# Kernel optimization log

Measured on AMD Instinct MI355X. Metric: run time of the kernel, lower is better.

## Reference

```python
import jax, jax.numpy as jnp
import numpy as np

B, C, H, W = 4, 64, 64, 64  # x shape; mask is (B,1,8H,8W)


def _conv(x, w, pad=0):
    return jax.lax.conv_general_dilated(
        x, w, (1, 1), [(pad, pad), (pad, pad)],
        dimension_numbers=('NCHW', 'OIHW', 'NCHW'))


def _inorm(x, eps=1e-5):  # InstanceNorm2d, affine=False, biased var (torch default)
    mu = x.mean(axis=(2, 3), keepdims=True)
    var = x.var(axis=(2, 3), keepdims=True)
    return (x - mu) * jax.lax.rsqrt(var + eps)


def _forward(x, mask, kconv_w1, kconv_w2, fs_w1, fs_w2, fs_b2, fs_fuse_w):
    b, c, h, w = x.shape
    n = h * w
    # MaxPool2d(8,8) then binarize
    m = jax.lax.reduce_window(mask, -jnp.inf, jax.lax.max,
                              (1, 1, 8, 8), (1, 1, 8, 8), 'VALID')
    m = (m > 0).astype(x.dtype)
    back = 1.0 - m
    # ResidualBlock K_conv (shared for K and Q paths in original code)
    y = jax.nn.relu(_inorm(_conv(x, kconv_w1, pad=1)))
    y = _inorm(_conv(y, kconv_w2, pad=1))
    kx = jax.nn.relu(y + x)
    # L2-normalized K/Q over channel dim
    K = (kx * back).reshape(b, c, n)
    K = K / (jnp.linalg.norm(K, axis=1, keepdims=True) + 1e-8)
    Q = (kx * m).reshape(b, c, n)
    Q = Q / (jnp.linalg.norm(Q, axis=1, keepdims=True) + 1e-8)
    V = (x * back).reshape(b, c, n)
    # cosine-similarity score map, temperature 20
    score = jnp.einsum('bcq,bck->bqk', Q, K) * 20.0  # (b, n_q, n_k)
    qm = m.reshape(b, 1, n)      # query mask (foreground)
    km = back.reshape(b, 1, n)   # key mask (background)
    NEG = -1000000.0
    validx = score + (1.0 - km) * NEG + (1.0 - qm.transpose(0, 2, 1)) * NEG
    att = jax.nn.softmax(validx, axis=-1) * (qm.transpose(0, 2, 1) * km)
    # att_fore[b,c,q] = sum_k V[b,c,k] * att[b,q,k]
    att_fore = jnp.einsum('bck,bqk->bcq', V, att).reshape(b, c, h, w)
    # Fusion_score
    feat1 = _conv(jnp.concatenate([x * m, att_fore * m], axis=1), fs_w1)
    s = jax.nn.sigmoid(_conv(feat1, fs_w2) + fs_b2[None, :, None, None])
    fused = _conv(jnp.concatenate([x * m, att_fore * m * (1.0 - s)], axis=1), fs_fuse_w)
    fs_out = fused * m + x * (1.0 - m)
    out = fs_out * m + x * (1.0 - m)
    # visualization attention mask
    visatt = att.sum(axis=1).reshape(b, 1, h, w)
    attmask = jnp.repeat(jnp.repeat(visatt, 8, axis=2), 8, axis=3)  # nearest upsample x8
    attmask = attmask / attmask.max()
    return out, attmask


def setup_inputs() -> dict:
    key = jax.random.key(0)
    ks = jax.random.split(key, 8)

    def wgt(k, shape, fan_in):
        return jax.random.normal(k, shape, jnp.float32) / np.sqrt(fan_in)

    x = jax.random.normal(ks[0], (B, C, H, W), jnp.float32)
    # sparse foreground mask so maxpool(8x8)>0 yields a mixed fg/bg mask
    mask = (jax.random.uniform(ks[1], (B, 1, H * 8, W * 8)) < 0.01).astype(jnp.float32)
    return dict(
        x=x, mask=mask,
        kconv_w1=wgt(ks[2], (C, C, 3, 3), C * 9),
        kconv_w2=wgt(ks[3], (C, C, 3, 3), C * 9),
        fs_w1=wgt(ks[4], (C, 2 * C, 1, 1), 2 * C),
        fs_w2=wgt(ks[5], (C, C, 1, 1), C),
        fs_b2=jnp.zeros((C,), jnp.float32),
        fs_fuse_w=wgt(ks[6], (C, 2 * C, 1, 1), 2 * C),
    )


def reference(x, mask, kconv_w1, kconv_w2, fs_w1, fs_w2, fs_b2, fs_fuse_w):
    return _forward(x, mask, kconv_w1, kconv_w2, fs_w1, fs_w2, fs_b2, fs_fuse_w)
```

## Files before the change

### kernel.cpp

```cpp
#include <hip/hip_runtime.h>
#include <hip/hip_bf16.h>

typedef __hip_bfloat16 bf16;
typedef __attribute__((ext_vector_type(8))) short short8;
typedef __attribute__((ext_vector_type(4))) float f32x4;
typedef __attribute__((ext_vector_type(16))) float f32x16;

#define BB 4
#define CC 64
#define NN 4096
#define MH 512
#define MW 512
#define LS 72

#define WB_AFC  ((size_t)0)
#define WB_DEN  ((size_t)4194304)
#define WB_VIS  ((size_t)4259840)
#define WB_QIX  ((size_t)4325376)
#define WB_KIX  ((size_t)4390912)
#define WB_MFL  ((size_t)4456448)
#define WB_CNT  ((size_t)4472832)
#define WB_STAT ((size_t)4472896)
#define WB_WT1  ((size_t)4476992)
#define WB_WT2  ((size_t)4550720)
#define WB_WFB  ((size_t)4624448)
#define WB_XT   ((size_t)8388608)
#define WB_KXT  ((size_t)10485760)
#define WB_E    ((size_t)16777216)
#define EB_ELEM ((size_t)8388608)

__device__ __forceinline__ float b2f(bf16 v) { return __bfloat162float(v); }
__device__ __forceinline__ float us2f(unsigned short u) { return __uint_as_float(((unsigned)u) << 16); }
__device__ __forceinline__ unsigned short f2bu(float f) {
  bf16 h = __float2bfloat16(f);
  return *(unsigned short*)&h;
}

__global__ __launch_bounds__(256) void k_pre(const float* __restrict__ x,
                                             const float* __restrict__ mask,
                                             const float* __restrict__ w1,
                                             const float* __restrict__ w2,
                                             const float* __restrict__ fw1,
                                             const float* __restrict__ fw2,
                                             const float* __restrict__ fwf,
                                             float* __restrict__ outp,
                                             unsigned short* __restrict__ xt,
                                             unsigned char* __restrict__ mfl,
                                             float* __restrict__ vis,
                                             float* __restrict__ gstat,
                                             unsigned int* __restrict__ vmaxb,
                                             unsigned short* __restrict__ wT1,
                                             unsigned short* __restrict__ wT2,
                                             unsigned short* __restrict__ wfb) {
  __shared__ float lx[64][65];
  int t = threadIdx.x;
  if (blockIdx.x < 256) {
    int b = blockIdx.x >> 6, p0 = (blockIdx.x & 63) * 64;
    const float* xb = x + (size_t)b * CC * NN + p0;
    float* ob = outp + (size_t)b * CC * NN + p0;
    for (int idx = t; idx < 4096; idx += 256) {
      int c = idx >> 6, j = idx & 63;
      float v = xb[c * NN + j];
      lx[j][c] = v;
      ob[c * NN + j] = v;
    }
    __syncthreads();
    unsigned short* xo = xt + ((size_t)b * NN + p0) * 64;
    for (int idx = t; idx < 2048; idx += 256) {
      int j = idx >> 5, c2 = (idx & 31) * 2;
      ushort2 w2v;
      w2v.x = f2bu(lx[j][c2]);
      w2v.y = f2bu(lx[j][c2 + 1]);
      *(ushort2*)&xo[j * 64 + c2] = w2v;
    }
  } else {
    int g = (blockIdx.x - 256) * 256 + t;
    int o = g >> 2, sub = g & 3;
    int b = o >> 12, p = o & 4095;
    int py = p >> 6, px = p & 63;
    const float* mb = mask + (size_t)b * MH * MW + (py * 8 + sub * 2) * MW + px * 8;
    float mx = 0.f;
    #pragma unroll
    for (int dy = 0; dy < 2; ++dy) {
      const float4* r4 = (const float4*)(mb + dy * MW);
      float4 a = r4[0], c = r4[1];
      mx = fmaxf(mx, fmaxf(fmaxf(a.x, a.y), fmaxf(a.z, a.w)));
      mx = fmaxf(mx, fmaxf(fmaxf(c.x, c.y), fmaxf(c.z, c.w)));
    }
    mx = fmaxf(mx, __shfl_xor(mx, 1));
    mx = fmaxf(mx, __shfl_xor(mx, 2));
    if (sub == 0) {
      mfl[o] = (mx > 0.f) ? 1 : 0;
      vis[o] = 0.f;
    }
    if (g < 1024) gstat[g] = 0.f;
    if (g == 0) vmaxb[0] = 0u;
    if (g < 36864) {
      int tap = g >> 12;
      int rem = g & 4095;
      int co = rem >> 6, ci = rem & 63;
      int src = (co * 64 + ci) * 9 + tap;
      wT1[g] = f2bu(w1[src]);
      wT2[g] = f2bu(w2[src]);
    } else if (g < 57344) {
      int j2 = g - 36864;
      if (j2 < 8192)       wfb[j2] = f2bu(fw1[j2]);
      else if (j2 < 12288) wfb[j2] = f2bu(fw2[j2 - 8192]);
      else                 wfb[j2] = f2bu(fwf[j2 - 12288]);
    }
  }
}

__global__ __launch_bounds__(256) void k_compact(const unsigned char* __restrict__ mfl,
                                                 int* __restrict__ qidx, int* __restrict__ kidx,
                                                 int* __restrict__ nq, int* __restrict__ nk) {
  int b = blockIdx.x;
  __shared__ unsigned char lm[4096];
  int t = threadIdx.x;
  *(uint4*)&lm[t * 16] = *(const uint4*)&mfl[b * NN + t * 16];
  __syncthreads();
  if (t >= 64) return;
  int lane = t;
  int qb = 0, kb = 0;
  #pragma unroll
  for (int it = 0; it < 64; ++it) {
    int p = it * 64 + lane;
    bool f = lm[p] != 0;
    unsigned long long bal = __ballot(f);
    int before = __popcll(bal & ((1ULL << lane) - 1ULL));
    if (f)  qidx[b * NN + qb + before] = p;
    if (!f) kidx[b * NN + kb + (lane - before)] = p;
    int cnt = __popcll(bal);
    qb += cnt; kb += 64 - cnt;
  }
  if (lane == 0) { nq[b] = qb; nk[b] = kb; }
}

template <bool NORM_IN>
__global__ __launch_bounds__(256) void k_convm(const unsigned short* __restrict__ src,
                                               const unsigned short* __restrict__ wT,
                                               const float* __restrict__ insum,
                                               const float* __restrict__ insq,
                                               unsigned short* __restrict__ dst,
                                               float* __restrict__ gsum,
                                               float* __restrict__ gsq) {
  int b = blockIdx.y;
  int r = blockIdx.x;
  __shared__ unsigned short bx[198 * LS];
  __shared__ float nmean[64], ninv[64];
  int t = threadIdx.x;
  if (NORM_IN) {
    if (t < 64) {
      float m = insum[b * 64 + t] * (1.f / NN);
      float v = fmaxf(insq[b * 64 + t] * (1.f / NN) - m * m, 0.f);
      nmean[t] = m; ninv[t] = rsqrtf(v + 1e-5f);
    }
    __syncthreads();
  }
  const unsigned short* sb = src + (size_t)b * NN * 64;
  for (int idx = t; idx < 198 * 8; idx += 256) {
    int row = idx >> 3, c8 = (idx & 7) * 8;
    int dy = row / 66;
    int cx = row - dy * 66 - 1;
    int rr = r + dy - 1;
    uint4 v = make_uint4(0u, 0u, 0u, 0u);
    if ((unsigned)rr < 64u && (unsigned)cx < 64u) {
      v = *(const uint4*)(sb + ((size_t)(rr * 64 + cx)) * 64 + c8);
      if (NORM_IN) {
        unsigned short* e = (unsigned short*)&v;
        #pragma unroll
        for (int j = 0; j < 8; ++j)
          e[j] = f2bu(fmaxf((us2f(e[j]) - nmean[c8 + j]) * ninv[c8 + j], 0.f));
      }
    }
    *(uint4*)&bx[row * LS + c8] = v;
  }
  __syncthreads();
  int lane = t & 63;
  int quad = lane >> 4, col = lane & 15;
  int qw = (t >> 6) * 16;
  f32x4 acc[4] = {{0.f,0.f,0.f,0.f},{0.f,0.f,0.f,0.f},{0.f,0.f,0.f,0.f},{0.f,0.f,0.f,0.f}};
  #pragma unroll
  for (int tap = 0; tap < 9; ++tap) {
    int dy = tap / 3, dx = tap - dy * 3 - 1;
    const unsigned short* wrow = wT + ((size_t)tap * 64 + qw + col) * 64;
    short8 a0 = *(const short8*)(wrow + quad * 8);
    short8 a1 = *(const short8*)(wrow + 32 + quad * 8);
    int rbase = dy * 66 + dx + 1;
    #pragma unroll
    for (int nt = 0; nt < 4; ++nt) {
      int row = rbase + nt * 16 + col;
      short8 b0 = *(const short8*)&bx[row * LS + quad * 8];
      short8 b1 = *(const short8*)&bx[row * LS + 32 + quad * 8];
      acc[nt] = __builtin_amdgcn_mfma_f32_16x16x32_bf16(a0, b0, acc[nt], 0, 0, 0);
      acc[nt] = __builtin_amdgcn_mfma_f32_16x16x32_bf16(a1, b1, acc[nt], 0, 0, 0);
    }
  }
  #pragma unroll
  for (int rr = 0; rr < 4; ++rr) {
    float s1 = acc[0][rr] + acc[1][rr] + acc[2][rr] + acc[3][rr];
    float s2 = acc[0][rr]*acc[0][rr] + acc[1][rr]*acc[1][rr]
             + acc[2][rr]*acc[2][rr] + acc[3][rr]*acc[3][rr];
    s1 += __shfl_xor(s1, 1); s2 += __shfl_xor(s2, 1);
    s1 += __shfl_xor(s1, 2); s2 += __shfl_xor(s2, 2);
    s1 += __shfl_xor(s1, 4); s2 += __shfl_xor(s2, 4);
    s1 += __shfl_xor(s1, 8); s2 += __shfl_xor(s2, 8);
    if (col == 0) {
      int co = qw + quad * 4 + rr;
      atomicAdd(&gsum[b * 64 + co], s1);
      atomicAdd(&gsq[b * 64 + co], s2);
    }
  }
  __syncthreads();
  #pragma unroll
  for (int nt = 0; nt < 4; ++nt)
    #pragma unroll
    for (int rr = 0; rr < 4; ++rr)
      bx[(nt * 16 + col) * LS + qw + quad * 4 + rr] = f2bu(acc[nt][rr]);
  __syncthreads();
  unsigned short* db = dst + ((size_t)b * NN + r * 64) * 64;
  for (int idx = t; idx < 512; idx += 256) {
    int px = idx >> 3, c8 = (idx & 7) * 8;
    *(uint4*)(db + (size_t)px * 64 + c8) = *(const uint4*)&bx[px * LS + c8];
  }
}

__global__ __launch_bounds__(256) void k_knorm(unsigned short* __restrict__ kxt,
                                               const unsigned short* __restrict__ xt,
                                               const float* __restrict__ gsum,
                                               const float* __restrict__ gsq,
                                               float* __restrict__ afc,
                                               float* __restrict__ den) {
  int b = blockIdx.x >> 6;
  int p0 = (blockIdx.x & 63) * 64;
  __shared__ float m2[64], i2[64];
  int t = threadIdx.x;
  if (t < 64) {
    float m = gsum[b * 64 + t] * (1.f / NN);
    float v = fmaxf(gsq[b * 64 + t] * (1.f / NN) - m * m, 0.f);
    m2[t] = m; i2[t] = rsqrtf(v + 1e-5f);
  }
  size_t gid = (size_t)blockIdx.x * 256 + t;
  float4 z4 = make_float4(0.f, 0.f, 0.f, 0.f);
  float4* az = (float4*)afc;
  #pragma unroll
  for (int j = 0; j < 4; ++j) az[gid + (size_t)j * 65536] = z4;
  if (gid < 16384) den[gid] = 0.f;
  __syncthreads();
  int px = t >> 2, c0 = (t & 3) * 16;
  size_t base = ((size_t)b * NN + p0 + px) * 64 + c0;
  unsigned short kv[16], xv[16];
  *(uint4*)&kv[0] = *(const uint4*)(kxt + base);
  *(uint4*)&kv[8] = *(const uint4*)(kxt + base + 8);
  *(uint4*)&xv[0] = *(const uint4*)(xt + base);
  *(uint4*)&xv[8] = *(const uint4*)(xt + base + 8);
  float v[16]; float ss = 0.f;
  #pragma unroll
  for (int j = 0; j < 16; ++j) {
    float f = fmaxf((us2f(kv[j]) - m2[c0 + j]) * i2[c0 + j] + us2f(xv[j]), 0.f);
    v[j] = f; ss += f * f;
  }
  ss += __shfl_xor(ss, 1);
  ss += __shfl_xor(ss, 2);
  float inv = 1.f / (sqrtf(ss) + 1e-8f);
  #pragma unroll
  for (int j = 0; j < 16; ++j) kv[j] = f2bu(v[j] * inv);
  *(uint4*)(kxt + base) = *(const uint4*)&kv[0];
  *(uint4*)(kxt + base + 8) = *(const uint4*)&kv[8];
}

__global__ __launch_bounds__(256) void k_att1(const unsigned short* __restrict__ khat,
                                              const unsigned short* __restrict__ xt,
                                              const int* __restrict__ qidx, const int* __restrict__ kidx,
                                              const int* __restrict__ nqv, const int* __restrict__ nkv,
                                              float* __restrict__ afc, float* __restrict__ den,
                                              unsigned short* __restrict__ eg) {
  int b = blockIdx.y;
  int nqb = nqv[b], nkb = nkv[b];
  int q0 = (blockIdx.x >> 3) * 64;
  int part = blockIdx.x & 7;
  if (q0 >= nqb) return;
  int ntiles = (nkb + 63) >> 6;
  int nt_blk = (part < ntiles) ? ((ntiles - part + 7) >> 3) : 0;
  if (nt_blk == 0) return;
  int NKP = (nkb + 63) & ~63;
  __shared__ unsigned short lk [64 * LS];
  __shared__ unsigned short lvT[64 * LS];
  __shared__ unsigned short le [64 * LS];
  __shared__ int lidxa[512];
  int t = threadIdx.x;
  int wave = t >> 6, lane = t & 63;
  int l31 = lane & 31, lhi = lane >> 5;
  int qh = wave >> 1, kh = wave & 1;
  const int* qix = qidx + b * NN;
  const int* kix = kidx + b * NN;
  const unsigned short* khb = khat + (size_t)b * NN * 64;
  const unsigned short* xtb = xt + (size_t)b * NN * 64;
  unsigned short* egb = eg + (size_t)b * EB_ELEM;
  int qq_a = q0 + qh * 32 + l31;
  int qp_a = (qq_a < nqb) ? qix[qq_a] : qix[0];
  short8 aq[4];
  #pragma unroll
  for (int ks = 0; ks < 4; ++ks)
    aq[ks] = *(const short8*)(khb + (size_t)qp_a * 64 + ks * 16 + lhi * 8);
  for (int idx = t; idx < nt_blk * 64; idx += 256) {
    int it = idx >> 6, k = idx & 63;
    lidxa[idx] = kix[(part + it * 8) * 64 + k];
  }
  __syncthreads();
  int klo = t >> 3, c8 = (t & 7) * 8, vcc = t & 7;
  uint4 g0, g1, g2, g3;
  auto issue_gather = [&](int it) {
    int j0 = (part + it * 8) * 64;
    const int* lp = lidxa + it * 64;
    uint4 z = make_uint4(0u, 0u, 0u, 0u);
    g0 = (j0 + klo      < nkb) ? *(const uint4*)(khb + (size_t)lp[klo] * 64 + c8) : z;
    g1 = (j0 + klo + 32 < nkb) ? *(const uint4*)(khb + (size_t)lp[klo + 32] * 64 + c8) : z;
    g2 = (j0 + 2 * klo     < nkb) ? *(const uint4*)(xtb + (size_t)lp[2 * klo] * 64 + c8) : z;
    g3 = (j0 + 2 * klo + 1 < nkb) ? *(const uint4*)(xtb + (size_t)lp[2 * klo + 1] * 64 + c8) : z;
  };
  issue_gather(0);
  f32x16 pv, dsum;
  #pragma unroll
  for (int i = 0; i < 16; ++i) { pv[i] = 0.f; dsum[i] = 0.f; }
  for (int it = 0; it < nt_blk; ++it) {
    int j0 = (part + it * 8) * 64;
    __syncthreads();
    *(uint4*)&lk[klo * LS + c8] = g0;
    *(uint4*)&lk[(klo + 32) * LS + c8] = g1;
    {
      const unsigned short* e0 = (const unsigned short*)&g2;
      const unsigned short* e1 = (const unsigned short*)&g3;
      int pbase = klo & 3, prun = klo >> 2;
      int pp = pbase + ((prun ^ vcc) << 2);
      #pragma unroll
      for (int jj = 0; jj < 8; ++jj) {
        unsigned int w2 = (unsigned)e0[jj] | ((unsigned)e1[jj] << 16);
        *(unsigned int*)&lvT[(c8 + jj) * LS + pp * 2] = w2;
      }
    }
    __syncthreads();
    if (it + 1 < nt_blk) issue_gather(it + 1);
    f32x16 s;
    #pragma unroll
    for (int i = 0; i < 16; ++i) s[i] = 0.f;
    #pragma unroll
    for (int ks = 0; ks < 4; ++ks) {
      short8 bk = *(const short8*)&lk[(kh * 32 + l31) * LS + ks * 16 + lhi * 8];
      s = __builtin_amdgcn_mfma_f32_32x32x16_bf16(aq[ks], bk, s, 0, 0, 0);
    }
    bool kval = (j0 + kh * 32 + l31) < nkb;
    #pragma unroll
    for (int reg = 0; reg < 16; ++reg) {
      float e = kval ? __expf(20.f * s[reg]) : 0.f;
      dsum[reg] += e;
      int row = (reg & 3) + 8 * (reg >> 2) + 4 * lhi;
      le[(qh * 32 + row) * LS + kh * 32 + l31] = f2bu(e);
    }
    __syncthreads();
    for (int idx = t; idx < 512; idx += 256) {
      int q = idx >> 3, cc8 = (idx & 7) * 8;
      if (q0 + q < nqb)
        *(uint4*)(egb + (size_t)(q0 + q) * NKP + j0 + cc8) = *(const uint4*)&le[q * LS + cc8];
    }
    int c = kh * 32 + l31;
    int c37 = (c >> 3) & 7;
    #pragma unroll
    for (int ks = 0; ks < 4; ++ks) {
      short8 a  = *(const short8*)&le[(qh * 32 + l31) * LS + ks * 16 + lhi * 8];
      int run = ks * 2 + lhi;
      short8 bv = *(const short8*)&lvT[c * LS + ((run ^ c37) << 3)];
      pv = __builtin_amdgcn_mfma_f32_32x32x16_bf16(a, bv, pv, 0, 0, 0);
    }
  }
  #pragma unroll
  for (int reg = 0; reg < 16; ++reg) {
    float v = dsum[reg];
    v += __shfl_xor(v, 1); v += __shfl_xor(v, 2); v += __shfl_xor(v, 4);
    v += __shfl_xor(v, 8); v += __shfl_xor(v, 16);
    int row = (reg & 3) + 8 * (reg >> 2) + 4 * lhi;
    int qq = q0 + qh * 32 + row;
    if (l31 == 0 && qq < nqb) atomicAdd(&den[b * NN + qq], v);
  }
  #pragma unroll
  for (int reg = 0; reg < 16; ++reg) {
    int row = (reg & 3) + 8 * (reg >> 2) + 4 * lhi;
    int qq = q0 + qh * 32 + row;
    if (qq < nqb) atomicAdd(&afc[((size_t)b * NN + qq) * 64 + kh * 32 + l31], pv[reg]);
  }
}

__global__ __launch_bounds__(256) void k_vis(const unsigned short* __restrict__ eg,
                                             const float* __restrict__ den,
                                             const int* __restrict__ kidx,
                                             const int* __restrict__ nqv, const int* __restrict__ nkv,
                                             float* __restrict__ vis) {
  int b = blockIdx.z;
  int nqb = nqv[b], nkb = nkv[b];
  int k0 = blockIdx.x * 256;
  if (k0 >= nkb) return;
  int NKP = (nkb + 63) & ~63;
  int qpart = blockIdx.y;
  int qbeg = (qpart * nqb) >> 3;
  int qend = ((qpart + 1) * nqb) >> 3;
  __shared__ float wd[256];
  int t = threadIdx.x;
  int k = k0 + t;
  const unsigned short* eb = eg + (size_t)b * EB_ELEM;
  float acc = 0.f;
  for (int qc = qbeg; qc < qend; qc += 256) {
    __syncthreads();
    int qq = qc + t;
    float d = (qq < qend) ? den[b * NN + qq] : 0.f;
    wd[t] = (d > 0.f) ? 1.f / d : 0.f;
    __syncthreads();
    int lim = min(256, qend - qc);
    if (k < nkb) {
      const unsigned short* ep = eb + (size_t)qc * NKP + k;
      int j = 0;
      for (; j + 8 <= lim; j += 8) {
        #pragma unroll
        for (int u = 0; u < 8; ++u)
          acc += us2f(ep[(size_t)(j + u) * NKP]) * wd[j + u];
      }
      for (; j < lim; ++j)
        acc += us2f(ep[(size_t)j * NKP]) * wd[j];
    }
  }
  if (k < nkb) atomicAdd(&vis[b * NN + kidx[b * NN + k]], acc);
}

#define FS 136
__global__ __launch_bounds__(256) void k_fusionm(const unsigned short* __restrict__ xt,
                                                 const float* __restrict__ afc,
                                                 const float* __restrict__ den,
                                                 const int* __restrict__ qidx, const int* __restrict__ nqv,
                                                 const unsigned short* __restrict__ wall,
                                                 const float* __restrict__ b2,
                                                 float* __restrict__ outp) {
  int b = blockIdx.y;
  int nqb = nqv[b];
  int q0 = blockIdx.x * 64;
  if (q0 >= nqb) return;
  __shared__ unsigned short pxa[64 * FS];
  __shared__ unsigned short f1s[64 * LS];
  __shared__ int qpl[64];
  int t = threadIdx.x;
  int lane = t & 63;
  int quad = lane >> 4, col = lane & 15;
  int cb = (t >> 6) * 16;
  const int* qix = qidx + b * NN;
  const unsigned short* xtb = xt + (size_t)b * NN * 64;
  const unsigned short* w1b = wall;
  const unsigned short* w2b = wall + 8192;
  const unsigned short* wfb = wall + 12288;
  short8 a1[4], a2[2], af[4];
  #pragma unroll
  for (int kt = 0; kt < 4; ++kt) {
    a1[kt] = *(const short8*)&w1b[(cb + col) * 128 + kt * 32 + quad * 8];
    af[kt] = *(const short8*)&wfb[(cb + col) * 128 + kt * 32 + quad * 8];
  }
  #pragma unroll
  for (int kt = 0; kt < 2; ++kt)
    a2[kt] = *(const short8*)&w2b[(cb + col) * 64 + kt * 32 + quad * 8];
  float b2v[4];
  #pragma unroll
  for (int r = 0; r < 4; ++r) b2v[r] = b2[cb + quad * 4 + r];
  if (t < 64) qpl[t] = (q0 + t < nqb) ? qix[q0 + t] : -1;
  for (int idx = t; idx < 512; idx += 256) {
    int q = idx >> 3, c8 = (idx & 7) * 8;
    int qq = q0 + q;
    uint4 pv = make_uint4(0u, 0u, 0u, 0u);
    unsigned short pa8[8] = {0, 0, 0, 0, 0, 0, 0, 0};
    if (qq < nqb) {
      int qp = qix[qq];
      pv = *(const uint4*)(xtb + (size_t)qp * 64 + c8);
      float d = den[b * NN + qq];
      float invd = (d > 0.f) ? 1.f / d : 0.f;
      const float* ap = afc + ((size_t)b * NN + qq) * 64 + c8;
      #pragma unroll
      for (int j = 0; j < 8; ++j) pa8[j] = f2bu(ap[j] * invd);
    }
    *(uint4*)&pxa[q * FS + c8] = pv;
    *(uint4*)&pxa[q * FS + 64 + c8] = *(const uint4*)&pa8[0];
  }
  __syncthreads();
  #pragma unroll
  for (int qt = 0; qt < 4; ++qt) {
    f32x4 acc = {0.f, 0.f, 0.f, 0.f};
    #pragma unroll
    for (int kt = 0; kt < 4; ++kt) {
      short8 bfrag = *(const short8*)&pxa[(qt * 16 + col) * FS + kt * 32 + quad * 8];
      acc = __builtin_amdgcn_mfma_f32_16x16x32_bf16(a1[kt], bfrag, acc, 0, 0, 0);
    }
    #pragma unroll
    for (int r = 0; r < 4; ++r)
      f1s[(qt * 16 + col) * LS + cb + quad * 4 + r] = f2bu(acc[r]);
  }
  __syncthreads();
  #pragma unroll
  for (int qt = 0; qt < 4; ++qt) {
    f32x4 acc = {0.f, 0.f, 0.f, 0.f};
    #pragma unroll
    for (int kt = 0; kt < 2; ++kt) {
      short8 bfrag = *(const short8*)&f1s[(qt * 16 + col) * LS + kt * 32 + quad * 8];
      acc = __builtin_amdgcn_mfma_f32_16x16x32_bf16(a2[kt], bfrag, acc, 0, 0, 0);
    }
    #pragma unroll
    for (int r = 0; r < 4; ++r) {
      float sg = 1.f / (1.f + __expf(-(acc[r] + b2v[r])));
      int addr = (qt * 16 + col) * FS + 64 + cb + quad * 4 + r;
      pxa[addr] = f2bu(us2f(pxa[addr]) * (1.f - sg));
    }
  }
  __syncthreads();
  #pragma unroll
  for (int qt = 0; qt < 4; ++qt) {
    f32x4 acc = {0.f, 0.f, 0.f, 0.f};
    #pragma unroll
    for (int kt = 0; kt < 4; ++kt) {
      short8 bfrag = *(const short8*)&pxa[(qt * 16 + col) * FS + kt * 32 + quad * 8];
      acc = __builtin_amdgcn_mfma_f32_16x16x32_bf16(af[kt], bfrag, acc, 0, 0, 0);
    }
    int qp = qpl[qt * 16 + col];
    if (qp >= 0) {
      #pragma unroll
      for (int r = 0; r < 4; ++r)
        outp[((size_t)b * CC + cb + quad * 4 + r) * NN + qp] = acc[r];
    }
  }
}

__global__ __launch_bounds__(256) void k_vmax(const float* __restrict__ vis, unsigned int* __restrict__ vmaxb) {
  int i = blockIdx.x * 256 + threadIdx.x;
  float v = vis[i];
  #pragma unroll
  for (int off = 32; off > 0; off >>= 1) v = fmaxf(v, __shfl_down(v, off));
  if ((threadIdx.x & 63) == 0) atomicMax(vmaxb, __float_as_uint(v));
}

__global__ __launch_bounds__(256) void k_upsample(const float* __restrict__ vis,
                                                  const unsigned int* __restrict__ vmaxb,
                                                  float* __restrict__ out2) {
  int i = blockIdx.x * 256 + threadIdx.x;
  int b = i >> 18;
  int rem = i & 262143;
  int y = rem >> 9, x = rem & 511;
  float vm = __uint_as_float(vmaxb[0]);
  if (!(vm > 0.f)) vm = 1.f;
  out2[i] = vis[b * NN + (y >> 3) * 64 + (x >> 3)] / vm;
}

extern "C" void kernel_launch(void* const* d_in, const int* in_sizes, int n_in,
                              void* d_out, int out_size, void* d_ws, size_t ws_size,
                              hipStream_t stream) {
  const float* x    = (const float*)d_in[0];
  const float* mask = (const float*)d_in[1];
  const float* w1   = (const float*)d_in[2];
  const float* w2c  = (const float*)d_in[3];
  const float* fsw1 = (const float*)d_in[4];
  const float* fsw2 = (const float*)d_in[5];
  const float* fsb2 = (const float*)d_in[6];
  const float* fswf = (const float*)d_in[7];
  float* out = (float*)d_out;
  char* wsb = (char*)d_ws;

  float* afc = (float*)(wsb + WB_AFC);
  float* den = (float*)(wsb + WB_DEN);
  float* vis = (float*)(wsb + WB_VIS);
  int* qidx  = (int*)(wsb + WB_QIX);
  int* kidx  = (int*)(wsb + WB_KIX);
  unsigned char* mfl = (unsigned char*)(wsb + WB_MFL);
  int* nq = (int*)(wsb + WB_CNT);
  int* nk = nq + 4;
  unsigned int* vmaxb = (unsigned int*)(nq + 8);
  float* gstat = (float*)(wsb + WB_STAT);
  float* gsum1 = gstat;
  float* gsq1  = gstat + 256;
  float* gsum2 = gstat + 512;
  float* gsq2  = gstat + 768;
  unsigned short* wT1 = (unsigned short*)(wsb + WB_WT1);
  unsigned short* wT2 = (unsigned short*)(wsb + WB_WT2);
  unsigned short* wall = (unsigned short*)(wsb + WB_WFB);
  unsigned short* y1t = (unsigned short*)(wsb + WB_AFC);
  unsigned short* xt  = (unsigned short*)(wsb + WB_XT);
  unsigned short* kxt = (unsigned short*)(wsb + WB_KXT);
  unsigned short* khat = kxt;
  unsigned short* eg  = (unsigned short*)(wsb + WB_E);

  k_pre<<<512, 256, 0, stream>>>(x, mask, w1, w2c, fsw1, fsw2, fswf,
                                 out, xt, mfl, vis, gstat, vmaxb, wT1, wT2, wall);
  k_compact<<<4, 256, 0, stream>>>(mfl, qidx, kidx, nq, nk);
  k_convm<false><<<dim3(64, BB), 256, 0, stream>>>(xt, wT1, nullptr, nullptr, y1t, gsum1, gsq1);
  k_convm<true><<<dim3(64, BB), 256, 0, stream>>>(y1t, wT2, gsum1, gsq1, kxt, gsum2, gsq2);
  k_knorm<<<256, 256, 0, stream>>>(kxt, xt, gsum2, gsq2, afc, den);
  k_att1<<<dim3(512, BB), 256, 0, stream>>>(khat, xt, qidx, kidx, nq, nk, afc, den, eg);
  k_vis<<<dim3(16, 8, BB), 256, 0, stream>>>(eg, den, kidx, nq, nk, vis);
  k_fusionm<<<dim3(64, BB), 256, 0, stream>>>(xt, afc, den, qidx, nq, wall, fsb2, out);
  k_vmax<<<64, 256, 0, stream>>>(vis, vmaxb);
  k_upsample<<<4096, 256, 0, stream>>>(vis, vmaxb, out + 1048576);
}
```

Before: 184.6 us.

## Replace global atomic accumulations with per-partition partial buffers reduced by consumers

Conv instance-norm stats, attention numerators/denominators and visualization sums are now written to per-row or per-partition slices instead of accumulated with global atomicAdd. The consuming kernels sum the partials, which also removes the zero-init passes over afc/den. The upsample kernel is vectorized to write float4. This trades atomic contention and zeroing traffic for extra partial-buffer reads and more workspace memory.

```diff
diff --git a/kernel.cpp b/kernel.cpp
--- a/kernel.cpp
+++ b/kernel.cpp
@@ -14,22 +14,23 @@
 #define LS 72
 
 #define WB_AFC  ((size_t)0)
-#define WB_DEN  ((size_t)4194304)
-#define WB_VIS  ((size_t)4259840)
 #define WB_QIX  ((size_t)4325376)
 #define WB_KIX  ((size_t)4390912)
 #define WB_MFL  ((size_t)4456448)
 #define WB_CNT  ((size_t)4472832)
-#define WB_STAT ((size_t)4472896)
+#define WB_VIS  ((size_t)4259840)
 #define WB_WT1  ((size_t)4476992)
 #define WB_WT2  ((size_t)4550720)
 #define WB_WFB  ((size_t)4624448)
 #define WB_XT   ((size_t)8388608)
 #define WB_KXT  ((size_t)10485760)
 #define WB_E    ((size_t)16777216)
-#define EB_ELEM ((size_t)8388608)
-
-__device__ __forceinline__ float b2f(bf16 v) { return __bfloat162float(v); }
+#define EB_ELEM ((size_t)16777216)
+#define WB_AFCP ((size_t)150994944)
+#define WB_DENP ((size_t)184549376)
+#define WB_VISP ((size_t)185597952)
+#define WB_GST  ((size_t)186122240)
+
 __device__ __forceinline__ float us2f(unsigned short u) { return __uint_as_float(((unsigned)u) << 16); }
 __device__ __forceinline__ unsigned short f2bu(float f) {
   bf16 h = __float2bfloat16(f);
@@ -47,7 +48,6 @@
                                              unsigned short* __restrict__ xt,
                                              unsigned char* __restrict__ mfl,
                                              float* __restrict__ vis,
-                                             float* __restrict__ gstat,
                                              unsigned int* __restrict__ vmaxb,
                                              unsigned short* __restrict__ wT1,
                                              unsigned short* __restrict__ wT2,
@@ -93,7 +93,6 @@
       mfl[o] = (mx > 0.f) ? 1 : 0;
       vis[o] = 0.f;
     }
-    if (g < 1024) gstat[g] = 0.f;
     if (g == 0) vmaxb[0] = 0u;
     if (g < 36864) {
       int tap = g >> 12;
@@ -142,8 +141,8 @@
                                                const float* __restrict__ insum,
                                                const float* __restrict__ insq,
                                                unsigned short* __restrict__ dst,
-                                               float* __restrict__ gsum,
-                                               float* __restrict__ gsq) {
+                                               float* __restrict__ gsump,
+                                               float* __restrict__ gsqp) {
   int b = blockIdx.y;
   int r = blockIdx.x;
   __shared__ unsigned short bx[198 * LS];
@@ -151,8 +150,14 @@
   int t = threadIdx.x;
   if (NORM_IN) {
     if (t < 64) {
-      float m = insum[b * 64 + t] * (1.f / NN);
-      float v = fmaxf(insq[b * 64 + t] * (1.f / NN) - m * m, 0.f);
+      float s = 0.f, s2v = 0.f;
+      #pragma unroll 8
+      for (int r2 = 0; r2 < 64; ++r2) {
+        s   += insum[((size_t)r2 * BB + b) * 64 + t];
+        s2v += insq [((size_t)r2 * BB + b) * 64 + t];
+      }
+      float m = s * (1.f / NN);
+      float v = fmaxf(s2v * (1.f / NN) - m * m, 0.f);
       nmean[t] = m; ninv[t] = rsqrtf(v + 1e-5f);
     }
     __syncthreads();
@@ -207,8 +212,8 @@
     s1 += __shfl_xor(s1, 8); s2 += __shfl_xor(s2, 8);
     if (col == 0) {
       int co = qw + quad * 4 + rr;
-      atomicAdd(&gsum[b * 64 + co], s1);
-      atomicAdd(&gsq[b * 64 + co], s2);
+      gsump[((size_t)r * BB + b) * 64 + co] = s1;
+      gsqp [((size_t)r * BB + b) * 64 + co] = s2;
     }
   }
   __syncthreads();
@@ -227,25 +232,23 @@
 
 __global__ __launch_bounds__(256) void k_knorm(unsigned short* __restrict__ kxt,
                                                const unsigned short* __restrict__ xt,
-                                               const float* __restrict__ gsum,
-                                               const float* __restrict__ gsq,
-                                               float* __restrict__ afc,
-                                               float* __restrict__ den) {
+                                               const float* __restrict__ gsump,
+                                               const float* __restrict__ gsqp) {
   int b = blockIdx.x >> 6;
   int p0 = (blockIdx.x & 63) * 64;
   __shared__ float m2[64], i2[64];
   int t = threadIdx.x;
   if (t < 64) {
-    float m = gsum[b * 64 + t] * (1.f / NN);
-    float v = fmaxf(gsq[b * 64 + t] * (1.f / NN) - m * m, 0.f);
+    float s = 0.f, s2v = 0.f;
+    #pragma unroll 8
+    for (int r2 = 0; r2 < 64; ++r2) {
+      s   += gsump[((size_t)r2 * BB + b) * 64 + t];
+      s2v += gsqp [((size_t)r2 * BB + b) * 64 + t];
+    }
+    float m = s * (1.f / NN);
+    float v = fmaxf(s2v * (1.f / NN) - m * m, 0.f);
     m2[t] = m; i2[t] = rsqrtf(v + 1e-5f);
   }
-  size_t gid = (size_t)blockIdx.x * 256 + t;
-  float4 z4 = make_float4(0.f, 0.f, 0.f, 0.f);
-  float4* az = (float4*)afc;
-  #pragma unroll
-  for (int j = 0; j < 4; ++j) az[gid + (size_t)j * 65536] = z4;
-  if (gid < 16384) den[gid] = 0.f;
   __syncthreads();
   int px = t >> 2, c0 = (t & 3) * 16;
   size_t base = ((size_t)b * NN + p0 + px) * 64 + c0;
@@ -273,7 +276,7 @@
                                               const unsigned short* __restrict__ xt,
                                               const int* __restrict__ qidx, const int* __restrict__ kidx,
                                               const int* __restrict__ nqv, const int* __restrict__ nkv,
-                                              float* __restrict__ afc, float* __restrict__ den,
+                                              float* __restrict__ afc_part, float* __restrict__ den_part,
                                               unsigned short* __restrict__ eg) {
   int b = blockIdx.y;
   int nqb = nqv[b], nkb = nkv[b];
@@ -282,7 +285,6 @@
   if (q0 >= nqb) return;
   int ntiles = (nkb + 63) >> 6;
   int nt_blk = (part < ntiles) ? ((ntiles - part + 7) >> 3) : 0;
-  if (nt_blk == 0) return;
   int NKP = (nkb + 63) & ~63;
   __shared__ unsigned short lk [64 * LS];
   __shared__ unsigned short lvT[64 * LS];
@@ -297,6 +299,8 @@
   const unsigned short* khb = khat + (size_t)b * NN * 64;
   const unsigned short* xtb = xt + (size_t)b * NN * 64;
   unsigned short* egb = eg + (size_t)b * EB_ELEM;
+  float* afcp = afc_part + (((size_t)part * BB + b) * NN) * 64;
+  float* denp = den_part + (((size_t)(part * 2 + kh)) * BB + b) * NN;
   int qq_a = q0 + qh * 32 + l31;
   int qp_a = (qq_a < nqb) ? qix[qq_a] : qix[0];
   short8 aq[4];
@@ -319,7 +323,7 @@
     g2 = (j0 + 2 * klo     < nkb) ? *(const uint4*)(xtb + (size_t)lp[2 * klo] * 64 + c8) : z;
     g3 = (j0 + 2 * klo + 1 < nkb) ? *(const uint4*)(xtb + (size_t)lp[2 * klo + 1] * 64 + c8) : z;
   };
-  issue_gather(0);
+  if (nt_blk > 0) issue_gather(0);
   f32x16 pv, dsum;
   #pragma unroll
   for (int i = 0; i < 16; ++i) { pv[i] = 0.f; dsum[i] = 0.f; }
@@ -380,21 +384,20 @@
     v += __shfl_xor(v, 8); v += __shfl_xor(v, 16);
     int row = (reg & 3) + 8 * (reg >> 2) + 4 * lhi;
     int qq = q0 + qh * 32 + row;
-    if (l31 == 0 && qq < nqb) atomicAdd(&den[b * NN + qq], v);
+    if (l31 == 0 && qq < nqb) denp[qq] = v;
   }
   #pragma unroll
   for (int reg = 0; reg < 16; ++reg) {
     int row = (reg & 3) + 8 * (reg >> 2) + 4 * lhi;
     int qq = q0 + qh * 32 + row;
-    if (qq < nqb) atomicAdd(&afc[((size_t)b * NN + qq) * 64 + kh * 32 + l31], pv[reg]);
+    if (qq < nqb) afcp[(size_t)qq * 64 + kh * 32 + l31] = pv[reg];
   }
 }
 
 __global__ __launch_bounds__(256) void k_vis(const unsigned short* __restrict__ eg,
-                                             const float* __restrict__ den,
-                                             const int* __restrict__ kidx,
+                                             const float* __restrict__ den_part,
                                              const int* __restrict__ nqv, const int* __restrict__ nkv,
-                                             float* __restrict__ vis) {
+                                             float* __restrict__ visp) {
   int b = blockIdx.z;
   int nqb = nqv[b], nkb = nkv[b];
   int k0 = blockIdx.x * 256;
@@ -411,7 +414,11 @@
   for (int qc = qbeg; qc < qend; qc += 256) {
     __syncthreads();
     int qq = qc + t;
-    float d = (qq < qend) ? den[b * NN + qq] : 0.f;
+    float d = 0.f;
+    if (qq < qend) {
+      #pragma unroll
+      for (int p2 = 0; p2 < 16; ++p2) d += den_part[((size_t)p2 * BB + b) * NN + qq];
+    }
     wd[t] = (d > 0.f) ? 1.f / d : 0.f;
     __syncthreads();
     int lim = min(256, qend - qc);
@@ -427,13 +434,13 @@
         acc += us2f(ep[(size_t)j * NKP]) * wd[j];
     }
   }
-  if (k < nkb) atomicAdd(&vis[b * NN + kidx[b * NN + k]], acc);
+  if (k < nkb) visp[((size_t)qpart * BB + b) * NN + k] = acc;
 }
 
 #define FS 136
 __global__ __launch_bounds__(256) void k_fusionm(const unsigned short* __restrict__ xt,
-                                                 const float* __restrict__ afc,
-                                                 const float* __restrict__ den,
+                                                 const float* __restrict__ afc_part,
+                                                 const float* __restrict__ den_part,
                                                  const int* __restrict__ qidx, const int* __restrict__ nqv,
                                                  const unsigned short* __restrict__ wall,
                                                  const float* __restrict__ b2,
@@ -475,11 +482,23 @@
     if (qq < nqb) {
       int qp = qix[qq];
       pv = *(const uint4*)(xtb + (size_t)qp * 64 + c8);
-      float d = den[b * NN + qq];
+      float d = 0.f;
+      #pragma unroll
+      for (int p2 = 0; p2 < 16; ++p2)
+        d += den_part[((size_t)p2 * BB + b) * NN + qq];
+      float av[8];
+      #pragma unroll
+      for (int j = 0; j < 8; ++j) av[j] = 0.f;
+      #pragma unroll
+      for (int p2 = 0; p2 < 8; ++p2) {
+        const float4* ap4 = (const float4*)(afc_part + (((size_t)p2 * BB + b) * NN + qq) * 64 + c8);
+        float4 u0 = ap4[0], u1 = ap4[1];
+        av[0] += u0.x; av[1] += u0.y; av[2] += u0.z; av[3] += u0.w;
+        av[4] += u1.x; av[5] += u1.y; av[6] += u1.z; av[7] += u1.w;
+      }
       float invd = (d > 0.f) ? 1.f / d : 0.f;
-      const float* ap = afc + ((size_t)b * NN + qq) * 64 + c8;
       #pragma unroll
-      for (int j = 0; j < 8; ++j) pa8[j] = f2bu(ap[j] * invd);
+      for (int j = 0; j < 8; ++j) pa8[j] = f2bu(av[j] * invd);
     }
     *(uint4*)&pxa[q * FS + c8] = pv;
     *(uint4*)&pxa[q * FS + 64 + c8] = *(const uint4*)&pa8[0];
@@ -531,9 +550,19 @@
   }
 }
 
-__global__ __launch_bounds__(256) void k_vmax(const float* __restrict__ vis, unsigned int* __restrict__ vmaxb) {
+__global__ __launch_bounds__(256) void k_vmax(const float* __restrict__ visp,
+                                              const int* __restrict__ kidx,
+                                              const int* __restrict__ nkv,
+                                              float* __restrict__ vis,
+                                              unsigned int* __restrict__ vmaxb) {
   int i = blockIdx.x * 256 + threadIdx.x;
-  float v = vis[i];
+  int b = i >> 12, k = i & 4095;
+  float v = 0.f;
+  if (k < nkv[b]) {
+    #pragma unroll
+    for (int p2 = 0; p2 < 8; ++p2) v += visp[((size_t)p2 * BB + b) * NN + k];
+    vis[b * NN + kidx[b * NN + k]] = v;
+  }
   #pragma unroll
   for (int off = 32; off > 0; off >>= 1) v = fmaxf(v, __shfl_down(v, off));
   if ((threadIdx.x & 63) == 0) atomicMax(vmaxb, __float_as_uint(v));
@@ -542,13 +571,14 @@
 __global__ __launch_bounds__(256) void k_upsample(const float* __restrict__ vis,
                                                   const unsigned int* __restrict__ vmaxb,
                                                   float* __restrict__ out2) {
-  int i = blockIdx.x * 256 + threadIdx.x;
-  int b = i >> 18;
-  int rem = i & 262143;
-  int y = rem >> 9, x = rem & 511;
+  int i4 = blockIdx.x * 256 + threadIdx.x;
+  int b = i4 >> 16;
+  int rem = i4 & 65535;
+  int y = rem >> 7, x4 = (rem & 127) * 4;
   float vm = __uint_as_float(vmaxb[0]);
   if (!(vm > 0.f)) vm = 1.f;
-  out2[i] = vis[b * NN + (y >> 3) * 64 + (x >> 3)] / vm;
+  float v = vis[b * NN + (y >> 3) * 64 + (x4 >> 3)] / vm;
+  ((float4*)out2)[i4] = make_float4(v, v, v, v);
 }
 
 extern "C" void kernel_launch(void* const* d_in, const int* in_sizes, int n_in,
@@ -565,8 +595,6 @@
   float* out = (float*)d_out;
   char* wsb = (char*)d_ws;
 
-  float* afc = (float*)(wsb + WB_AFC);
-  float* den = (float*)(wsb + WB_DEN);
   float* vis = (float*)(wsb + WB_VIS);
   int* qidx  = (int*)(wsb + WB_QIX);
   int* kidx  = (int*)(wsb + WB_KIX);
@@ -574,11 +602,6 @@
   int* nq = (int*)(wsb + WB_CNT);
   int* nk = nq + 4;
   unsigned int* vmaxb = (unsigned int*)(nq + 8);
-  float* gstat = (float*)(wsb + WB_STAT);
-  float* gsum1 = gstat;
-  float* gsq1  = gstat + 256;
-  float* gsum2 = gstat + 512;
-  float* gsq2  = gstat + 768;
   unsigned short* wT1 = (unsigned short*)(wsb + WB_WT1);
   unsigned short* wT2 = (unsigned short*)(wsb + WB_WT2);
   unsigned short* wall = (unsigned short*)(wsb + WB_WFB);
@@ -587,16 +610,23 @@
   unsigned short* kxt = (unsigned short*)(wsb + WB_KXT);
   unsigned short* khat = kxt;
   unsigned short* eg  = (unsigned short*)(wsb + WB_E);
+  float* afc_part = (float*)(wsb + WB_AFCP);
+  float* den_part = (float*)(wsb + WB_DENP);
+  float* visp     = (float*)(wsb + WB_VISP);
+  float* gsum1p = (float*)(wsb + WB_GST);
+  float* gsq1p  = (float*)(wsb + WB_GST + 65536);
+  float* gsum2p = (float*)(wsb + WB_GST + 131072);
+  float* gsq2p  = (float*)(wsb + WB_GST + 196608);
 
   k_pre<<<512, 256, 0, stream>>>(x, mask, w1, w2c, fsw1, fsw2, fswf,
-                                 out, xt, mfl, vis, gstat, vmaxb, wT1, wT2, wall);
+                                 out, xt, mfl, vis, vmaxb, wT1, wT2, wall);
   k_compact<<<4, 256, 0, stream>>>(mfl, qidx, kidx, nq, nk);
-  k_convm<false><<<dim3(64, BB), 256, 0, stream>>>(xt, wT1, nullptr, nullptr, y1t, gsum1, gsq1);
-  k_convm<true><<<dim3(64, BB), 256, 0, stream>>>(y1t, wT2, gsum1, gsq1, kxt, gsum2, gsq2);
-  k_knorm<<<256, 256, 0, stream>>>(kxt, xt, gsum2, gsq2, afc, den);
-  k_att1<<<dim3(512, BB), 256, 0, stream>>>(khat, xt, qidx, kidx, nq, nk, afc, den, eg);
-  k_vis<<<dim3(16, 8, BB), 256, 0, stream>>>(eg, den, kidx, nq, nk, vis);
-  k_fusionm<<<dim3(64, BB), 256, 0, stream>>>(xt, afc, den, qidx, nq, wall, fsb2, out);
-  k_vmax<<<64, 256, 0, stream>>>(vis, vmaxb);
-  k_upsample<<<4096, 256, 0, stream>>>(vis, vmaxb, out + 1048576);
-}
+  k_convm<false><<<dim3(64, BB), 256, 0, stream>>>(xt, wT1, nullptr, nullptr, y1t, gsum1p, gsq1p);
+  k_convm<true><<<dim3(64, BB), 256, 0, stream>>>(y1t, wT2, gsum1p, gsq1p, kxt, gsum2p, gsq2p);
+  k_knorm<<<256, 256, 0, stream>>>(kxt, xt, gsum2p, gsq2p);
+  k_att1<<<dim3(512, BB), 256, 0, stream>>>(khat, xt, qidx, kidx, nq, nk, afc_part, den_part, eg);
+  k_vis<<<dim3(16, 8, BB), 256, 0, stream>>>(eg, den_part, nq, nk, visp);
+  k_fusionm<<<dim3(64, BB), 256, 0, stream>>>(xt, afc_part, den_part, qidx, nq, wall, fsb2, out);
+  k_vmax<<<64, 256, 0, stream>>>(visp, kidx, nk, vis, vmaxb);
+  k_upsample<<<1024, 256, 0, stream>>>(vis, vmaxb, out + 1048576);
+}
```

Result: faster. 174.6 us (-5.4%).
